# Performance work log

Hardware: AMD Instinct MI355X
Metric: run time of the kernel (lower is better)

## Reference

```python
import jax, jax.numpy as jnp
import numpy as np

DT = 0.001  # forward-arg default in the original module
EPS = 1e-10


def setup_inputs() -> dict:
    key = jax.random.key(0)
    k1, k2 = jax.random.split(key)
    x = jax.random.normal(k1, (5000, 512, 16), dtype=jnp.float32)  # [nt, traces, channels]
    y = jax.random.normal(k2, (5000, 512, 16), dtype=jnp.float32)
    return {"x": x, "y": y}


def reference(x, y):
    # Per-(t,c) L2 norms over time axis (dim 0): shape [T, C]
    xnorm = jnp.linalg.norm(x, ord=2, axis=0) + EPS
    ynorm = jnp.linalg.norm(y, ord=2, axis=0) + EPS
    # Per-(t,c) dot products over time: shape [T, C]
    dots = jnp.einsum('ntc,ntc->tc', x, y)
    # cc = -dot(xn * dt, yn) = -dt * dot(x, y) / (||x|| * ||y||)
    cc = -DT * dots / (xnorm * ynorm)
    # Original skips slices where max|x| == 0 (contributes 0.0)
    mask = jnp.max(jnp.abs(x), axis=0) > 0
    return jnp.sum(jnp.where(mask, cc, jnp.zeros_like(cc)))
```

## Files before the change

kernel.cpp:

```cpp
#include <hip/hip_runtime.h>
#include <hip/hip_bf16.h>
#include <math.h>


#define NT       5000
#define NROW_F   8192
#define NCOL     8192
#define NCOL4    2048

typedef __attribute__((address_space(3))) void lds_void;
typedef const __attribute__((address_space(1))) void gm_void;

__global__ __launch_bounds__(256) void ncc_partial(const float* __restrict__ xg,
                                                   const float* __restrict__ yg,
                                                   float4* __restrict__ ws,
                                                   int clen, int nchunk, int T) {
    __shared__ float4 BA[4][4][2][64];
    __shared__ float4 BB[4][4][2][64];

    const int tid  = threadIdx.x;
    const int w    = tid >> 6;
    const int lane = tid & 63;
    const int bx   = blockIdx.x;
    const int ch   = blockIdx.y;
    const int n0   = ch * clen;
    int n1 = n0 + clen; if (n1 > NT) n1 = NT;

    const int colf = bx * 1024 + tid * 4;

    float4 sxx = make_float4(0.f, 0.f, 0.f, 0.f);
    float4 syy = make_float4(0.f, 0.f, 0.f, 0.f);
    float4 sxy = make_float4(0.f, 0.f, 0.f, 0.f);
    float4 mx  = make_float4(0.f, 0.f, 0.f, 0.f);

#define ACC4(a, b)                                                      \
    sxx.x = fmaf(a.x, a.x, sxx.x); sxx.y = fmaf(a.y, a.y, sxx.y);       \
    sxx.z = fmaf(a.z, a.z, sxx.z); sxx.w = fmaf(a.w, a.w, sxx.w);       \
    syy.x = fmaf(b.x, b.x, syy.x); syy.y = fmaf(b.y, b.y, syy.y);       \
    syy.z = fmaf(b.z, b.z, syy.z); syy.w = fmaf(b.w, b.w, syy.w);       \
    sxy.x = fmaf(a.x, b.x, sxy.x); sxy.y = fmaf(a.y, b.y, sxy.y);       \
    sxy.z = fmaf(a.z, b.z, sxy.z); sxy.w = fmaf(a.w, b.w, sxy.w);       \
    mx.x = fmaxf(mx.x, fabsf(a.x)); mx.y = fmaxf(mx.y, fabsf(a.y));     \
    mx.z = fmaxf(mx.z, fabsf(a.z)); mx.w = fmaxf(mx.w, fabsf(a.w))

#define ISSUE(BUF, t)                                                         \
    {                                                                         \
        _Pragma("unroll")                                                     \
        for (int r = 0; r < 4; ++r) {                                         \
            int n = n0 + (t) * 4 + r;                                         \
            if (n > NT - 1) n = NT - 1;                                       \
            const float* px = xg + (size_t)n * NROW_F + colf;                 \
            const float* py = yg + (size_t)n * NROW_F + colf;                 \
            __builtin_amdgcn_global_load_lds((gm_void*)px,                    \
                (lds_void*)&BUF[w][r][0][0], 16, 0, 0);                       \
            __builtin_amdgcn_global_load_lds((gm_void*)py,                    \
                (lds_void*)&BUF[w][r][1][0], 16, 0, 0);                       \
        }                                                                     \
    }

#define COMPUTE(BUF, t)                                                       \
    {                                                                         \
        _Pragma("unroll")                                                     \
        for (int r = 0; r < 4; ++r) {                                         \
            float4 a = BUF[w][r][0][lane];                                    \
            float4 b = BUF[w][r][1][lane];                                    \
            int n = n0 + (t) * 4 + r;                                         \
            if (n < n1) { ACC4(a, b); }                                       \
        }                                                                     \
    }

#define WAITV(N)                                                              \
    asm volatile("s_waitcnt vmcnt(" #N ")" ::: "memory");                     \
    __builtin_amdgcn_sched_barrier(0)

#define WAITL()                                                               \
    asm volatile("s_waitcnt lgkmcnt(0)" ::: "memory");                        \
    __builtin_amdgcn_sched_barrier(0)

    ISSUE(BA, 0);
    ISSUE(BB, 1);
    for (int t = 0; t + 4 <= T; t += 2) {
        WAITV(8);
        COMPUTE(BA, t);
        WAITL();
        ISSUE(BA, t + 2);
        WAITV(8);
        COMPUTE(BB, t + 1);
        WAITL();
        ISSUE(BB, t + 3);
    }
    WAITV(8);
    COMPUTE(BA, T - 2);
    WAITV(0);
    COMPUTE(BB, T - 1);

#undef ACC4
#undef ISSUE
#undef COMPUTE
#undef WAITV
#undef WAITL

    float4* SXX = ws;
    float4* SYY = ws + (size_t)nchunk * NCOL4;
    float4* SXY = ws + (size_t)2 * nchunk * NCOL4;
    float4* MX  = ws + (size_t)3 * nchunk * NCOL4;
    const size_t idx = (size_t)ch * NCOL4 + bx * 256 + tid;
    SXX[idx] = sxx;
    SYY[idx] = syy;
    SXY[idx] = sxy;
    MX[idx]  = mx;
}

__global__ __launch_bounds__(256) void ncc_combine(const float4* __restrict__ ws4,
                                                   float* __restrict__ partials,
                                                   int nchunk) {
    const int c4l   = threadIdx.x & 15;
    const int strip = threadIdx.x >> 4;
    const int c4    = blockIdx.x * 16 + c4l;

    const float4* SXX = ws4;
    const float4* SYY = ws4 + (size_t)nchunk * NCOL4;
    const float4* SXY = ws4 + (size_t)2 * nchunk * NCOL4;
    const float4* MX  = ws4 + (size_t)3 * nchunk * NCOL4;

    const int spc = (nchunk + 15) >> 4;
    int ch0 = strip * spc;
    int ch1 = ch0 + spc;
    if (ch1 > nchunk) ch1 = nchunk;

    float4 sxx = make_float4(0.f, 0.f, 0.f, 0.f);
    float4 syy = make_float4(0.f, 0.f, 0.f, 0.f);
    float4 sxy = make_float4(0.f, 0.f, 0.f, 0.f);
    float4 mx  = make_float4(0.f, 0.f, 0.f, 0.f);
    for (int ch = ch0; ch < ch1; ++ch) {
        const size_t idx = (size_t)ch * NCOL4 + c4;
        float4 a = SXX[idx], b = SYY[idx], d = SXY[idx], m = MX[idx];
        sxx.x += a.x; sxx.y += a.y; sxx.z += a.z; sxx.w += a.w;
        syy.x += b.x; syy.y += b.y; syy.z += b.z; syy.w += b.w;
        sxy.x += d.x; sxy.y += d.y; sxy.z += d.z; sxy.w += d.w;
        mx.x = fmaxf(mx.x, m.x); mx.y = fmaxf(mx.y, m.y);
        mx.z = fmaxf(mx.z, m.z); mx.w = fmaxf(mx.w, m.w);
    }

    __shared__ float4 L[16][4][16];
    L[strip][0][c4l] = sxx;
    L[strip][1][c4l] = syy;
    L[strip][2][c4l] = sxy;
    L[strip][3][c4l] = mx;
    __syncthreads();

    for (int s = 8; s >= 1; s >>= 1) {
        if (strip < s) {
            float4 a0 = L[strip][0][c4l], a1 = L[strip + s][0][c4l];
            float4 b0 = L[strip][1][c4l], b1 = L[strip + s][1][c4l];
            float4 d0 = L[strip][2][c4l], d1 = L[strip + s][2][c4l];
            float4 m0 = L[strip][3][c4l], m1 = L[strip + s][3][c4l];
            a0.x += a1.x; a0.y += a1.y; a0.z += a1.z; a0.w += a1.w;
            b0.x += b1.x; b0.y += b1.y; b0.z += b1.z; b0.w += b1.w;
            d0.x += d1.x; d0.y += d1.y; d0.z += d1.z; d0.w += d1.w;
            m0.x = fmaxf(m0.x, m1.x); m0.y = fmaxf(m0.y, m1.y);
            m0.z = fmaxf(m0.z, m1.z); m0.w = fmaxf(m0.w, m1.w);
            L[strip][0][c4l] = a0;
            L[strip][1][c4l] = b0;
            L[strip][2][c4l] = d0;
            L[strip][3][c4l] = m0;
        }
        __syncthreads();
    }

    if (strip == 0) {
        sxx = L[0][0][c4l];
        syy = L[0][1][c4l];
        sxy = L[0][2][c4l];
        mx  = L[0][3][c4l];
        float cc = 0.f;
        if (mx.x > 0.f) cc += -0.001f * sxy.x / ((sqrtf(sxx.x) + 1e-10f) * (sqrtf(syy.x) + 1e-10f));
        if (mx.y > 0.f) cc += -0.001f * sxy.y / ((sqrtf(sxx.y) + 1e-10f) * (sqrtf(syy.y) + 1e-10f));
        if (mx.z > 0.f) cc += -0.001f * sxy.z / ((sqrtf(sxx.z) + 1e-10f) * (sqrtf(syy.z) + 1e-10f));
        if (mx.w > 0.f) cc += -0.001f * sxy.w / ((sqrtf(sxx.w) + 1e-10f) * (sqrtf(syy.w) + 1e-10f));
        for (int off = 8; off > 0; off >>= 1)
            cc += __shfl_down(cc, off);
        if (c4l == 0)
            partials[blockIdx.x] = cc;
    }
}

__global__ __launch_bounds__(128) void ncc_final(const float* __restrict__ partials,
                                                 float* __restrict__ out) {
    float v = partials[threadIdx.x];
    for (int off = 32; off > 0; off >>= 1)
        v += __shfl_down(v, off);
    __shared__ float r[2];
    if ((threadIdx.x & 63) == 0) r[threadIdx.x >> 6] = v;
    __syncthreads();
    if (threadIdx.x == 0) out[0] = r[0] + r[1];
}

extern "C" void kernel_launch(void* const* d_in, const int* in_sizes, int n_in,
                              void* d_out, int out_size, void* d_ws, size_t ws_size,
                              hipStream_t stream) {
    const float* x = (const float*)d_in[0];
    const float* y = (const float*)d_in[1];
    float* out = (float*)d_out;
    float* ws  = (float*)d_ws;

    const size_t per_chunk_bytes = 4ull * NCOL * sizeof(float);
    size_t avail = (ws_size > 1024) ? (ws_size - 1024) : 0;
    int nchunk = (int)(avail / per_chunk_bytes);
    if (nchunk > 64) nchunk = 64;
    if (nchunk < 1)  nchunk = 1;
    const int clen = (NT + nchunk - 1) / nchunk;

    int T = (clen + 3) / 4;
    if (T & 1) T++;
    if (T < 2) T = 2;

    float* partials = ws + 4ull * (size_t)nchunk * NCOL;

    dim3 g1(8, nchunk);
    ncc_partial<<<g1, 256, 0, stream>>>(x, y, (float4*)ws, clen, nchunk, T);
    ncc_combine<<<128, 256, 0, stream>>>((const float4*)ws, partials, nchunk);
    ncc_final<<<1, 128, 0, stream>>>(partials, out);
}
```

Before: 64.49 us.

## Fuse final reduction into combine via last-block atomic counter, fix chunk count

Removes the separate single-block final kernel: each combine block bumps an agent-scope atomic counter and the last block to arrive sums the 128 partials and writes the output. The chunk count is fixed at 32 instead of being derived from workspace size (up to 64), which halves the partial grid's parallelism and changes per-block work. The counter is reset inside the first partial kernel. The goal is to save one launch; the cost is fewer partial blocks and an atomic handshake.

```diff
diff --git a/kernel.cpp b/kernel.cpp
--- a/kernel.cpp
+++ b/kernel.cpp
@@ -7,6 +7,8 @@
 #define NROW_F   8192
 #define NCOL     8192
 #define NCOL4    2048
+#define NCHUNK   32
+#define NCBLK    128
 
 typedef __attribute__((address_space(3))) void lds_void;
 typedef const __attribute__((address_space(1))) void gm_void;
@@ -14,7 +16,8 @@
 __global__ __launch_bounds__(256) void ncc_partial(const float* __restrict__ xg,
                                                    const float* __restrict__ yg,
                                                    float4* __restrict__ ws,
-                                                   int clen, int nchunk, int T) {
+                                                   int* __restrict__ counter,
+                                                   int clen, int T) {
     __shared__ float4 BA[4][4][2][64];
     __shared__ float4 BB[4][4][2][64];
 
@@ -25,6 +28,8 @@
     const int ch   = blockIdx.y;
     const int n0   = ch * clen;
     int n1 = n0 + clen; if (n1 > NT) n1 = NT;
+
+    if (bx == 0 && ch == 0 && tid == 0) *counter = 0;
 
     const int colf = bx * 1024 + tid * 4;
 
@@ -101,9 +106,9 @@
 #undef WAITL
 
     float4* SXX = ws;
-    float4* SYY = ws + (size_t)nchunk * NCOL4;
-    float4* SXY = ws + (size_t)2 * nchunk * NCOL4;
-    float4* MX  = ws + (size_t)3 * nchunk * NCOL4;
+    float4* SYY = ws + (size_t)NCHUNK * NCOL4;
+    float4* SXY = ws + (size_t)2 * NCHUNK * NCOL4;
+    float4* MX  = ws + (size_t)3 * NCHUNK * NCOL4;
     const size_t idx = (size_t)ch * NCOL4 + bx * 256 + tid;
     SXX[idx] = sxx;
     SYY[idx] = syy;
@@ -113,20 +118,19 @@
 
 __global__ __launch_bounds__(256) void ncc_combine(const float4* __restrict__ ws4,
                                                    float* __restrict__ partials,
-                                                   int nchunk) {
+                                                   int* __restrict__ counter,
+                                                   float* __restrict__ out) {
     const int c4l   = threadIdx.x & 15;
     const int strip = threadIdx.x >> 4;
     const int c4    = blockIdx.x * 16 + c4l;
 
     const float4* SXX = ws4;
-    const float4* SYY = ws4 + (size_t)nchunk * NCOL4;
-    const float4* SXY = ws4 + (size_t)2 * nchunk * NCOL4;
-    const float4* MX  = ws4 + (size_t)3 * nchunk * NCOL4;
-
-    const int spc = (nchunk + 15) >> 4;
-    int ch0 = strip * spc;
-    int ch1 = ch0 + spc;
-    if (ch1 > nchunk) ch1 = nchunk;
+    const float4* SYY = ws4 + (size_t)NCHUNK * NCOL4;
+    const float4* SXY = ws4 + (size_t)2 * NCHUNK * NCOL4;
+    const float4* MX  = ws4 + (size_t)3 * NCHUNK * NCOL4;
+
+    const int ch0 = strip * (NCHUNK / 16);
+    const int ch1 = ch0 + (NCHUNK / 16);
 
     float4 sxx = make_float4(0.f, 0.f, 0.f, 0.f);
     float4 syy = make_float4(0.f, 0.f, 0.f, 0.f);
@@ -183,17 +187,27 @@
         if (c4l == 0)
             partials[blockIdx.x] = cc;
     }
-}
-
-__global__ __launch_bounds__(128) void ncc_final(const float* __restrict__ partials,
-                                                 float* __restrict__ out) {
-    float v = partials[threadIdx.x];
-    for (int off = 32; off > 0; off >>= 1)
-        v += __shfl_down(v, off);
-    __shared__ float r[2];
-    if ((threadIdx.x & 63) == 0) r[threadIdx.x >> 6] = v;
+
+    __shared__ int lastFlag;
+    if (threadIdx.x == 0) {
+        __threadfence();
+        int old = __hip_atomic_fetch_add(counter, 1, __ATOMIC_ACQ_REL,
+                                         __HIP_MEMORY_SCOPE_AGENT);
+        lastFlag = (old == NCBLK - 1);
+    }
     __syncthreads();
-    if (threadIdx.x == 0) out[0] = r[0] + r[1];
+    if (lastFlag) {
+        float v = 0.f;
+        if (threadIdx.x < NCBLK)
+            v = __hip_atomic_load(&partials[threadIdx.x], __ATOMIC_RELAXED,
+                                  __HIP_MEMORY_SCOPE_AGENT);
+        for (int off = 32; off > 0; off >>= 1)
+            v += __shfl_down(v, off);
+        __shared__ float r[4];
+        if ((threadIdx.x & 63) == 0) r[threadIdx.x >> 6] = v;
+        __syncthreads();
+        if (threadIdx.x == 0) out[0] = r[0] + r[1] + r[2] + r[3];
+    }
 }
 
 extern "C" void kernel_launch(void* const* d_in, const int* in_sizes, int n_in,
@@ -204,21 +218,15 @@
     float* out = (float*)d_out;
     float* ws  = (float*)d_ws;
 
-    const size_t per_chunk_bytes = 4ull * NCOL * sizeof(float);
-    size_t avail = (ws_size > 1024) ? (ws_size - 1024) : 0;
-    int nchunk = (int)(avail / per_chunk_bytes);
-    if (nchunk > 64) nchunk = 64;
-    if (nchunk < 1)  nchunk = 1;
-    const int clen = (NT + nchunk - 1) / nchunk;
-
+    const int clen = (NT + NCHUNK - 1) / NCHUNK;
     int T = (clen + 3) / 4;
     if (T & 1) T++;
     if (T < 2) T = 2;
 
-    float* partials = ws + 4ull * (size_t)nchunk * NCOL;
-
-    dim3 g1(8, nchunk);
-    ncc_partial<<<g1, 256, 0, stream>>>(x, y, (float4*)ws, clen, nchunk, T);
-    ncc_combine<<<128, 256, 0, stream>>>((const float4*)ws, partials, nchunk);
-    ncc_final<<<1, 128, 0, stream>>>(partials, out);
+    float* partials = ws + 4ull * NCHUNK * NCOL;
+    int*   counter  = (int*)(partials + NCBLK);
+
+    dim3 g1(8, NCHUNK);
+    ncc_partial<<<g1, 256, 0, stream>>>(x, y, (float4*)ws, counter, clen, T);
+    ncc_combine<<<NCBLK, 256, 0, stream>>>((const float4*)ws, partials, counter, out);
 }
```

Measured after the change: 66.22 us. +2.7%, slower.
